# Kernel optimization log

Measured on AMD Instinct MI355X. Metric: run time of the kernel, lower is better.

## Reference

```python
import jax, jax.numpy as jnp
import numpy as np

NUM_ITERATIONS = 3


def _squash_over_classes(s):
    # s: [B, C, O]; original squashes over dim=2 of [B,1,C,O,1] == the class dim C
    norm_sqr = jnp.sum(s * s, axis=1, keepdims=True)          # [B,1,O]
    scale = jnp.sqrt(norm_sqr) + 1e-10
    mag = norm_sqr / (1.0 + norm_sqr)
    return s * mag / scale


def setup_inputs() -> dict:
    key = jax.random.key(0)
    k1, k2 = jax.random.split(key)
    B, K, I, C, O = 256, 8, 1152, 10, 16
    x = jax.random.normal(k1, (B, K, I), dtype=jnp.float32)
    weights = jax.random.normal(k2, (I, C, O, K), dtype=jnp.float32)
    return {"x": x, "weights": weights}


def reference(x, weights):
    # x: [B, K, I]; weights: [I, C, O, K]
    B = x.shape[0]
    I, C = weights.shape[0], weights.shape[1]
    u = jnp.swapaxes(x, 1, 2)                                  # [B, I, K]
    # prediction vectors u_hat_{j|i}: [B, I, C, O]
    u_j_i = jnp.einsum('icok,bik->bico', weights, u)
    b = jnp.zeros((I, C), dtype=x.dtype)                       # routing logits (shared over batch)
    out = None
    for _ in range(NUM_ITERATIONS):
        c = jax.nn.softmax(b, axis=0)                          # softmax over input capsules I
        s = jnp.einsum('ic,bico->bco', c, u_j_i)               # weighted sum over I -> [B, C, O]
        out = _squash_over_classes(s)                          # [B, C, O]
        # agreement: <u_hat, v>, mean over batch -> [I, C]
        agr = jnp.einsum('bico,bco->ic', u_j_i, out) / B
        b = b + agr
    return out[..., None]                                      # [B, C, O, 1] matches out.squeeze(1)
```

## Files before the change

kernel.cpp:

```cpp
#include <hip/hip_runtime.h>

#define B 256
#define KDIM 8
#define IDIM 1152
#define CDIM 10
#define CO 160
#define IK 9216
#define NPART 6
#define AIT 6

typedef __bf16 bf16x8 __attribute__((ext_vector_type(8)));
typedef unsigned short ushort8 __attribute__((ext_vector_type(8)));
typedef float f32x4 __attribute__((ext_vector_type(4)));

__device__ __forceinline__ unsigned short f2bf(float f) {
  unsigned u = __float_as_uint(f);
  unsigned r = u + 0x7fff + ((u >> 16) & 1);
  return (unsigned short)(r >> 16);
}

union U8B8 { ushort8 u; bf16x8 h; };

__global__ void __launch_bounds__(256) k_prep(const float* __restrict__ x,
                                              const float* __restrict__ W,
                                              unsigned short* __restrict__ xtbT,
                                              unsigned short* __restrict__ xtkb,
                                              unsigned short* __restrict__ Wrb,
                                              float* __restrict__ logits) {
  __shared__ __align__(16) unsigned char smem[41280];
  const int bid = blockIdx.x;
  const int t = threadIdx.x;
  if (bid < 288) {
    float* tf = (float*)smem;
    const int i0 = (bid % 36) * 32;
    const int b0 = (bid / 36) * 32;
    const int tx = t & 31, ty = t >> 5;
#pragma unroll
    for (int r = 0; r < 4; ++r) {
      int b = b0 + ty + r * 8;
#pragma unroll
      for (int k = 0; k < 8; ++k)
        tf[k * 1056 + (ty + r * 8) * 33 + tx] =
            x[((size_t)b * KDIM + k) * IDIM + i0 + tx];
    }
    __syncthreads();
#pragma unroll
    for (int r = 0; r < 4; ++r) {
      int idx = r * 256 + t;
      int bb = idx >> 5, ii = idx & 31;
      ushort8 v;
#pragma unroll
      for (int k = 0; k < 8; ++k) v[k] = f2bf(tf[k * 1056 + bb * 33 + ii]);
      *reinterpret_cast<ushort8*>(&xtbT[(size_t)(b0 + bb) * IK + (i0 + ii) * 8]) = v;
    }
#pragma unroll
    for (int ii = 0; ii < 32; ++ii)
      xtkb[((size_t)(i0 + ii) * 8 + ty) * B + b0 + tx] =
          f2bf(tf[ty * 1056 + tx * 33 + ii]);
  } else {
    unsigned short* wt = (unsigned short*)smem;
    const int bz = bid - 288;
    const int i0 = bz * 16;
#pragma unroll
    for (int ii = 0; ii < 16; ++ii) {
      const float* src = &W[(size_t)(i0 + ii) * 1280];
#pragma unroll
      for (int p = 0; p < 5; ++p) {
        int j = p * 256 + t;
        wt[ii * 1288 + j] = f2bf(src[j]);
      }
    }
    __syncthreads();
#pragma unroll
    for (int p = 0; p < 10; ++p) {
      int idx = p * 256 + t;
      int co = idx >> 4, ii = idx & 15;
      ushort8 v = *reinterpret_cast<const ushort8*>(&wt[ii * 1288 + co * 8]);
      *reinterpret_cast<ushort8*>(&Wrb[(size_t)co * IK + (i0 + ii) * 8]) = v;
    }
    if (bz < 45) logits[bz * 256 + t] = 0.f;
  }
}

__global__ void __launch_bounds__(256) k_s(const float* __restrict__ logits,
                                           const unsigned short* __restrict__ Wrb,
                                           const unsigned short* __restrict__ xtbT,
                                           float* __restrict__ s_part) {
  const int c = blockIdx.x, bt4 = blockIdx.y, g = blockIdx.z;
  const int t = threadIdx.x, w = t >> 6, l = t & 63;
  const int lr = l & 15, lq = l >> 4;
  const int s = g * 4 + w;

  __shared__ float cls[IDIM];
  __shared__ float red4[4];
  __shared__ float red[3 * 1088];

  float m = -1e30f;
  for (int i = t; i < IDIM; i += 256) {
    float v = logits[i * CDIM + c];
    cls[i] = v;
    m = fmaxf(m, v);
  }
#pragma unroll
  for (int off = 32; off; off >>= 1) m = fmaxf(m, __shfl_xor(m, off));
  if ((t & 63) == 0) red4[t >> 6] = m;
  __syncthreads();
  m = fmaxf(fmaxf(red4[0], red4[1]), fmaxf(red4[2], red4[3]));
  __syncthreads();
  float ps = 0.f;
  for (int i = t; i < IDIM; i += 256) {
    float e = expf(cls[i] - m);
    cls[i] = e;
    ps += e;
  }
#pragma unroll
  for (int off = 32; off; off >>= 1) ps += __shfl_xor(ps, off);
  if ((t & 63) == 0) red4[t >> 6] = ps;
  __syncthreads();
  const float rinv = 1.f / (red4[0] + red4[1] + red4[2] + red4[3]);
  for (int i = t; i < IDIM; i += 256) cls[i] *= rinv;
  __syncthreads();

  f32x4 acc[4];
#pragma unroll
  for (int j = 0; j < 4; ++j) acc[j] = (f32x4){0.f, 0.f, 0.f, 0.f};

  const unsigned short* Ap  = &Wrb[((size_t)c * 16 + lr) * IK + lq * 8];
  const unsigned short* Bp0 = &xtbT[((size_t)(bt4 * 64 +  0 + lr)) * IK + lq * 8];
  const unsigned short* Bp1 = &xtbT[((size_t)(bt4 * 64 + 16 + lr)) * IK + lq * 8];
  const unsigned short* Bp2 = &xtbT[((size_t)(bt4 * 64 + 32 + lr)) * IK + lq * 8];
  const unsigned short* Bp3 = &xtbT[((size_t)(bt4 * 64 + 48 + lr)) * IK + lq * 8];

#pragma unroll 4
  for (int t9 = 0; t9 < 12; ++t9) {
    const int kc = s * 12 + t9;
    const int off = kc * 32;
    ushort8 av = *reinterpret_cast<const ushort8*>(Ap + off);
    float qv = cls[kc * 4 + lq];
    U8B8 b0; b0.u = *reinterpret_cast<const ushort8*>(Bp0 + off);
    U8B8 b1; b1.u = *reinterpret_cast<const ushort8*>(Bp1 + off);
    U8B8 b2; b2.u = *reinterpret_cast<const ushort8*>(Bp2 + off);
    U8B8 b3; b3.u = *reinterpret_cast<const ushort8*>(Bp3 + off);
    U8B8 a;
#pragma unroll
    for (int e = 0; e < 8; ++e) {
      float f = __uint_as_float((unsigned)av[e] << 16) * qv;
      a.u[e] = f2bf(f);
    }
    acc[0] = __builtin_amdgcn_mfma_f32_16x16x32_bf16(a.h, b0.h, acc[0], 0, 0, 0);
    acc[1] = __builtin_amdgcn_mfma_f32_16x16x32_bf16(a.h, b1.h, acc[1], 0, 0, 0);
    acc[2] = __builtin_amdgcn_mfma_f32_16x16x32_bf16(a.h, b2.h, acc[2], 0, 0, 0);
    acc[3] = __builtin_amdgcn_mfma_f32_16x16x32_bf16(a.h, b3.h, acc[3], 0, 0, 0);
  }

  if (w) {
#pragma unroll
    for (int j = 0; j < 4; ++j)
#pragma unroll
      for (int j2 = 0; j2 < 4; ++j2)
        red[(w - 1) * 1088 + l * 17 + j * 4 + j2] = acc[j][j2];
  }
  __syncthreads();
  if (w == 0) {
#pragma unroll
    for (int r = 0; r < 3; ++r)
#pragma unroll
      for (int j = 0; j < 4; ++j)
#pragma unroll
        for (int j2 = 0; j2 < 4; ++j2)
          acc[j][j2] += red[r * 1088 + l * 17 + j * 4 + j2];
#pragma unroll
    for (int j = 0; j < 4; ++j)
#pragma unroll
      for (int j2 = 0; j2 < 4; ++j2)
        s_part[((size_t)g * B + bt4 * 64 + j * 16 + lr) * CO + c * 16 + lq * 4 + j2] =
            acc[j][j2];
  }
}

__global__ void __launch_bounds__(256) k_sqm(const float* __restrict__ s_part,
                                             unsigned short* __restrict__ outT) {
  const int t = threadIdx.x;
  const int b0 = blockIdx.x * 8;
  __shared__ float sq[8][160];
  __shared__ float fo[8][16];
  float vv[8];
  if (t < CO) {
#pragma unroll
    for (int bi = 0; bi < 8; ++bi) {
      float sv = 0.f;
#pragma unroll
      for (int p = 0; p < NPART; ++p)
        sv += s_part[((size_t)p * B + b0 + bi) * CO + t];
      vv[bi] = sv;
      sq[bi][t] = sv * sv;
    }
  }
  __syncthreads();
  if (t < 128) {
    int bi = t >> 4, o = t & 15;
    float ns = 0.f;
#pragma unroll
    for (int c = 0; c < CDIM; ++c) ns += sq[bi][c * 16 + o];
    fo[bi][o] = (ns / (1.f + ns)) / (sqrtf(ns) + 1e-10f);
  }
  __syncthreads();
  if (t < CO) {
    ushort8 v;
#pragma unroll
    for (int bi = 0; bi < 8; ++bi) v[bi] = f2bf(vv[bi] * fo[bi][t & 15]);
    *reinterpret_cast<ushort8*>(&outT[(size_t)t * B + b0]) = v;
  }
}

__global__ void __launch_bounds__(256) k_sqf(const float* __restrict__ s_part,
                                             float* __restrict__ out) {
  const int t = threadIdx.x;
  const int b0 = blockIdx.x * 8;
  __shared__ float sq[8][160];
  __shared__ float fo[8][16];
  float vv[8];
  if (t < CO) {
#pragma unroll
    for (int bi = 0; bi < 8; ++bi) {
      float sv = 0.f;
#pragma unroll
      for (int p = 0; p < NPART; ++p)
        sv += s_part[((size_t)p * B + b0 + bi) * CO + t];
      vv[bi] = sv;
      sq[bi][t] = sv * sv;
    }
  }
  __syncthreads();
  if (t < 128) {
    int bi = t >> 4, o = t & 15;
    float ns = 0.f;
#pragma unroll
    for (int c = 0; c < CDIM; ++c) ns += sq[bi][c * 16 + o];
    fo[bi][o] = (ns / (1.f + ns)) / (sqrtf(ns) + 1e-10f);
  }
  __syncthreads();
  if (t < CO) {
#pragma unroll
    for (int bi = 0; bi < 8; ++bi)
      out[(size_t)(b0 + bi) * CO + t] = vv[bi] * fo[bi][t & 15];
  }
}

__global__ void __launch_bounds__(256) k_agr(const float* __restrict__ W,
                                             const unsigned short* __restrict__ xtkb,
                                             const unsigned short* __restrict__ outT,
                                             float* __restrict__ logits) {
  const int bx = blockIdx.x;
  const int bh = blockIdx.y;
  const int t = threadIdx.x, w = t >> 6, l = t & 63;
  const int lr = l & 15, lq = l >> 4;
  __shared__ __align__(16) float yl[CO][52];

  if (w < 3) {
    f32x4 acc[10];
#pragma unroll
    for (int nt = 0; nt < 10; ++nt) acc[nt] = (f32x4){0.f, 0.f, 0.f, 0.f};
    const unsigned short* Ap =
        &xtkb[(size_t)(bx * 48 + w * 16 + lr) * B + bh * 64 + lq * 8];
    const unsigned short* Bp = &outT[(size_t)lr * B + bh * 64 + lq * 8];
#pragma unroll
    for (int kc = 0; kc < 2; ++kc) {
      U8B8 a; a.u = *reinterpret_cast<const ushort8*>(Ap + kc * 32);
#pragma unroll
      for (int nt = 0; nt < 10; ++nt) {
        U8B8 bv;
        bv.u = *reinterpret_cast<const ushort8*>(Bp + (size_t)nt * 16 * B + kc * 32);
        acc[nt] = __builtin_amdgcn_mfma_f32_16x16x32_bf16(a.h, bv.h, acc[nt], 0, 0, 0);
      }
    }
#pragma unroll
    for (int nt = 0; nt < 10; ++nt)
#pragma unroll
      for (int j = 0; j < 4; ++j)
        yl[nt * 16 + lr][w * 16 + lq * 4 + j] = acc[nt][j];
  }
  __syncthreads();

  if (t < 120) {
    const int ii = t / 20, rem = t % 20, cc = rem >> 1, oh = rem & 1;
    const float* Wp = &W[((size_t)(bx * AIT + ii) * CDIM + cc) * 128 + oh * 64];
    float sum = 0.f;
#pragma unroll
    for (int o = 0; o < 8; ++o) {
      float4 w0 = *(const float4*)(&Wp[o * 8]);
      float4 w1 = *(const float4*)(&Wp[o * 8 + 4]);
      const float* yr = &yl[cc * 16 + oh * 8 + o][ii * 8];
      float4 y0 = *(const float4*)(&yr[0]);
      float4 y1 = *(const float4*)(&yr[4]);
      sum += w0.x * y0.x + w0.y * y0.y + w0.z * y0.z + w0.w * y0.w
           + w1.x * y1.x + w1.y * y1.y + w1.z * y1.z + w1.w * y1.w;
    }
    sum += __shfl_xor(sum, 1);
    if (oh == 0)
      atomicAdd(&logits[(bx * AIT + ii) * CDIM + cc], sum * (1.f / (float)B));
  }
}

extern "C" void kernel_launch(void* const* d_in, const int* in_sizes, int n_in,
                              void* d_out, int out_size, void* d_ws, size_t ws_size,
                              hipStream_t stream) {
  const float* x = (const float*)d_in[0];
  const float* W = (const float*)d_in[1];
  float* out = (float*)d_out;

  float* logits = (float*)d_ws;
  float* s_part = logits + IDIM * CDIM;
  unsigned short* xtbT = (unsigned short*)(s_part + (size_t)NPART * B * CO);
  unsigned short* xtkb = xtbT + (size_t)B * IK;
  unsigned short* Wrb  = xtkb + (size_t)IK * B;
  unsigned short* outT = Wrb + (size_t)CO * IK;

  k_prep<<<360, 256, 0, stream>>>(x, W, xtbT, xtkb, Wrb, logits);

  for (int it = 0; it < 3; ++it) {
    k_s<<<dim3(CDIM, 4, NPART), 256, 0, stream>>>(logits, Wrb, xtbT, s_part);
    if (it < 2) {
      k_sqm<<<32, 256, 0, stream>>>(s_part, outT);
      k_agr<<<dim3(IDIM / AIT, 4), 256, 0, stream>>>(W, xtkb, outT, logits);
    } else {
      k_sqf<<<32, 256, 0, stream>>>(s_part, out);
    }
  }
}
```

Before: 83.93 us.

## Pre-pack MFMA operands into fragment-contiguous layouts and specialize first-iteration uniform softmax

The prep kernel now writes x, W and the transposed x directly in a per-lane MFMA fragment order, so each wave's 64 lanes read one contiguous 1KB chunk instead of strided rows. The squash kernel writes its output in the matching packed layout for the agreement kernel. The first routing iteration uses a template specialization that skips the softmax, since the logits are zero and the weights are uniform at 1/I. The softmax weights are also hoisted into registers. The cost is more complex index math in the prep and squash kernels.

```diff
diff --git a/kernel.cpp b/kernel.cpp
--- a/kernel.cpp
+++ b/kernel.cpp
@@ -21,17 +21,17 @@
 
 union U8B8 { ushort8 u; bf16x8 h; };
 
+
 __global__ void __launch_bounds__(256) k_prep(const float* __restrict__ x,
                                               const float* __restrict__ W,
-                                              unsigned short* __restrict__ xtbT,
-                                              unsigned short* __restrict__ xtkb,
-                                              unsigned short* __restrict__ Wrb,
+                                              unsigned short* __restrict__ XbP,
+                                              unsigned short* __restrict__ XkP,
+                                              unsigned short* __restrict__ WqP,
                                               float* __restrict__ logits) {
-  __shared__ __align__(16) unsigned char smem[41280];
   const int bid = blockIdx.x;
   const int t = threadIdx.x;
   if (bid < 288) {
-    float* tf = (float*)smem;
+    __shared__ float tf[KDIM * 1056];
     const int i0 = (bid % 36) * 32;
     const int b0 = (bid / 36) * 32;
     const int tx = t & 31, ty = t >> 5;
@@ -47,96 +47,115 @@
 #pragma unroll
     for (int r = 0; r < 4; ++r) {
       int idx = r * 256 + t;
-      int bb = idx >> 5, ii = idx & 31;
+      int bth = idx >> 9, kc8 = (idx >> 6) & 7, lq = (idx >> 4) & 3, lr = idx & 15;
       ushort8 v;
 #pragma unroll
-      for (int k = 0; k < 8; ++k) v[k] = f2bf(tf[k * 1056 + bb * 33 + ii]);
-      *reinterpret_cast<ushort8*>(&xtbT[(size_t)(b0 + bb) * IK + (i0 + ii) * 8]) = v;
-    }
-#pragma unroll
-    for (int ii = 0; ii < 32; ++ii)
-      xtkb[((size_t)(i0 + ii) * 8 + ty) * B + b0 + tx] =
-          f2bf(tf[ty * 1056 + tx * 33 + ii]);
+      for (int e = 0; e < 8; ++e)
+        v[e] = f2bf(tf[e * 1056 + (bth * 16 + lr) * 33 + kc8 * 4 + lq]);
+      int bt = (b0 >> 4) + bth;
+      int kc = (i0 >> 2) + kc8;
+      *reinterpret_cast<ushort8*>(
+          &XbP[(((size_t)bt * 288 + kc) * 64 + lq * 16 + lr) * 8]) = v;
+    }
+    {
+      const int bh = b0 >> 6, kc = (b0 >> 5) & 1;
+#pragma unroll
+      for (int r = 0; r < 4; ++r) {
+        int idx = r * 256 + t;
+        int il = idx >> 5, k = (idx >> 2) & 7, lql = idx & 3;
+        int i = i0 + il;
+        int bx = i / 6, r6 = i - bx * 6;
+        int w = r6 >> 1, lr = (r6 & 1) * 8 + k;
+        ushort8 v;
+#pragma unroll
+        for (int e = 0; e < 8; ++e)
+          v[e] = f2bf(tf[k * 1056 + (lql * 8 + e) * 33 + il]);
+        *reinterpret_cast<ushort8*>(
+            &XkP[((((size_t)(bx * 3 + w) * 4 + bh) * 2 + kc) * 64 + lql * 16 + lr) * 8]) = v;
+      }
+    }
   } else {
-    unsigned short* wt = (unsigned short*)smem;
     const int bz = bid - 288;
     const int i0 = bz * 16;
-#pragma unroll
-    for (int ii = 0; ii < 16; ++ii) {
-      const float* src = &W[(size_t)(i0 + ii) * 1280];
-#pragma unroll
-      for (int p = 0; p < 5; ++p) {
-        int j = p * 256 + t;
-        wt[ii * 1288 + j] = f2bf(src[j]);
-      }
-    }
-    __syncthreads();
-#pragma unroll
-    for (int p = 0; p < 10; ++p) {
-      int idx = p * 256 + t;
-      int co = idx >> 4, ii = idx & 15;
-      ushort8 v = *reinterpret_cast<const ushort8*>(&wt[ii * 1288 + co * 8]);
-      *reinterpret_cast<ushort8*>(&Wrb[(size_t)co * IK + (i0 + ii) * 8]) = v;
+    const int ii = t >> 4, lr = t & 15;
+    const int i = i0 + ii;
+    const int kc = i >> 2, lq = i & 3;
+#pragma unroll
+    for (int c = 0; c < CDIM; ++c) {
+      const float* src = &W[(size_t)i * 1280 + c * 128 + lr * 8];
+      float4 w0 = *(const float4*)src;
+      float4 w1 = *(const float4*)(src + 4);
+      ushort8 v;
+      v[0] = f2bf(w0.x); v[1] = f2bf(w0.y); v[2] = f2bf(w0.z); v[3] = f2bf(w0.w);
+      v[4] = f2bf(w1.x); v[5] = f2bf(w1.y); v[6] = f2bf(w1.z); v[7] = f2bf(w1.w);
+      *reinterpret_cast<ushort8*>(
+          &WqP[(((size_t)c * 288 + kc) * 64 + lq * 16 + lr) * 8]) = v;
     }
     if (bz < 45) logits[bz * 256 + t] = 0.f;
   }
 }
 
+template <bool UNI>
 __global__ void __launch_bounds__(256) k_s(const float* __restrict__ logits,
-                                           const unsigned short* __restrict__ Wrb,
-                                           const unsigned short* __restrict__ xtbT,
+                                           const unsigned short* __restrict__ WqP,
+                                           const unsigned short* __restrict__ XbP,
                                            float* __restrict__ s_part) {
   const int c = blockIdx.x, bt4 = blockIdx.y, g = blockIdx.z;
   const int t = threadIdx.x, w = t >> 6, l = t & 63;
   const int lr = l & 15, lq = l >> 4;
   const int s = g * 4 + w;
 
-  __shared__ float cls[IDIM];
-  __shared__ float red4[4];
   __shared__ float red[3 * 1088];
 
-  float m = -1e30f;
-  for (int i = t; i < IDIM; i += 256) {
-    float v = logits[i * CDIM + c];
-    cls[i] = v;
-    m = fmaxf(m, v);
-  }
-#pragma unroll
-  for (int off = 32; off; off >>= 1) m = fmaxf(m, __shfl_xor(m, off));
-  if ((t & 63) == 0) red4[t >> 6] = m;
-  __syncthreads();
-  m = fmaxf(fmaxf(red4[0], red4[1]), fmaxf(red4[2], red4[3]));
-  __syncthreads();
-  float ps = 0.f;
-  for (int i = t; i < IDIM; i += 256) {
-    float e = expf(cls[i] - m);
-    cls[i] = e;
-    ps += e;
-  }
-#pragma unroll
-  for (int off = 32; off; off >>= 1) ps += __shfl_xor(ps, off);
-  if ((t & 63) == 0) red4[t >> 6] = ps;
-  __syncthreads();
-  const float rinv = 1.f / (red4[0] + red4[1] + red4[2] + red4[3]);
-  for (int i = t; i < IDIM; i += 256) cls[i] *= rinv;
-  __syncthreads();
+  float qreg[12];
+  if constexpr (UNI) {
+#pragma unroll
+    for (int t9 = 0; t9 < 12; ++t9) qreg[t9] = 1.f / (float)IDIM;
+  } else {
+    __shared__ float cls[IDIM];
+    __shared__ float red4[4];
+    float m = -1e30f;
+    for (int i = t; i < IDIM; i += 256) {
+      float v = logits[i * CDIM + c];
+      cls[i] = v;
+      m = fmaxf(m, v);
+    }
+#pragma unroll
+    for (int off = 32; off; off >>= 1) m = fmaxf(m, __shfl_xor(m, off));
+    if ((t & 63) == 0) red4[t >> 6] = m;
+    __syncthreads();
+    m = fmaxf(fmaxf(red4[0], red4[1]), fmaxf(red4[2], red4[3]));
+    __syncthreads();
+    float ps = 0.f;
+    for (int i = t; i < IDIM; i += 256) {
+      float e = expf(cls[i] - m);
+      cls[i] = e;
+      ps += e;
+    }
+#pragma unroll
+    for (int off = 32; off; off >>= 1) ps += __shfl_xor(ps, off);
+    if ((t & 63) == 0) red4[t >> 6] = ps;
+    __syncthreads();
+    const float rinv = 1.f / (red4[0] + red4[1] + red4[2] + red4[3]);
+#pragma unroll
+    for (int t9 = 0; t9 < 12; ++t9)
+      qreg[t9] = cls[(s * 12 + t9) * 4 + lq] * rinv;
+  }
 
   f32x4 acc[4];
 #pragma unroll
   for (int j = 0; j < 4; ++j) acc[j] = (f32x4){0.f, 0.f, 0.f, 0.f};
 
-  const unsigned short* Ap  = &Wrb[((size_t)c * 16 + lr) * IK + lq * 8];
-  const unsigned short* Bp0 = &xtbT[((size_t)(bt4 * 64 +  0 + lr)) * IK + lq * 8];
-  const unsigned short* Bp1 = &xtbT[((size_t)(bt4 * 64 + 16 + lr)) * IK + lq * 8];
-  const unsigned short* Bp2 = &xtbT[((size_t)(bt4 * 64 + 32 + lr)) * IK + lq * 8];
-  const unsigned short* Bp3 = &xtbT[((size_t)(bt4 * 64 + 48 + lr)) * IK + lq * 8];
+  const unsigned short* Ap  = &WqP[(size_t)c * 147456 + l * 8];
+  const unsigned short* Bp0 = &XbP[(size_t)(bt4 * 4 + 0) * 147456 + l * 8];
+  const unsigned short* Bp1 = &XbP[(size_t)(bt4 * 4 + 1) * 147456 + l * 8];
+  const unsigned short* Bp2 = &XbP[(size_t)(bt4 * 4 + 2) * 147456 + l * 8];
+  const unsigned short* Bp3 = &XbP[(size_t)(bt4 * 4 + 3) * 147456 + l * 8];
 
 #pragma unroll 4
   for (int t9 = 0; t9 < 12; ++t9) {
-    const int kc = s * 12 + t9;
-    const int off = kc * 32;
+    const int off = (s * 12 + t9) * 512;
     ushort8 av = *reinterpret_cast<const ushort8*>(Ap + off);
-    float qv = cls[kc * 4 + lq];
     U8B8 b0; b0.u = *reinterpret_cast<const ushort8*>(Bp0 + off);
     U8B8 b1; b1.u = *reinterpret_cast<const ushort8*>(Bp1 + off);
     U8B8 b2; b2.u = *reinterpret_cast<const ushort8*>(Bp2 + off);
@@ -144,7 +163,7 @@
     U8B8 a;
 #pragma unroll
     for (int e = 0; e < 8; ++e) {
-      float f = __uint_as_float((unsigned)av[e] << 16) * qv;
+      float f = __uint_as_float((unsigned)av[e] << 16) * qreg[t9];
       a.u[e] = f2bf(f);
     }
     acc[0] = __builtin_amdgcn_mfma_f32_16x16x32_bf16(a.h, b0.h, acc[0], 0, 0, 0);
@@ -179,7 +198,7 @@
 }
 
 __global__ void __launch_bounds__(256) k_sqm(const float* __restrict__ s_part,
-                                             unsigned short* __restrict__ outT) {
+                                             unsigned short* __restrict__ outP) {
   const int t = threadIdx.x;
   const int b0 = blockIdx.x * 8;
   __shared__ float sq[8][160];
@@ -206,10 +225,13 @@
   }
   __syncthreads();
   if (t < CO) {
+    const int nt = t >> 4, lr = t & 15;
+    const int bh = b0 >> 6, kc = (b0 >> 5) & 1, lq = (b0 >> 3) & 3;
     ushort8 v;
 #pragma unroll
     for (int bi = 0; bi < 8; ++bi) v[bi] = f2bf(vv[bi] * fo[bi][t & 15]);
-    *reinterpret_cast<ushort8*>(&outT[(size_t)t * B + b0]) = v;
+    *reinterpret_cast<ushort8*>(
+        &outP[((((size_t)bh * 10 + nt) * 2 + kc) * 4 + lq) * 128 + lr * 8]) = v;
   }
 }
 
@@ -248,8 +270,8 @@
 }
 
 __global__ void __launch_bounds__(256) k_agr(const float* __restrict__ W,
-                                             const unsigned short* __restrict__ xtkb,
-                                             const unsigned short* __restrict__ outT,
+                                             const unsigned short* __restrict__ XkP,
+                                             const unsigned short* __restrict__ outP,
                                              float* __restrict__ logits) {
   const int bx = blockIdx.x;
   const int bh = blockIdx.y;
@@ -261,16 +283,15 @@
     f32x4 acc[10];
 #pragma unroll
     for (int nt = 0; nt < 10; ++nt) acc[nt] = (f32x4){0.f, 0.f, 0.f, 0.f};
-    const unsigned short* Ap =
-        &xtkb[(size_t)(bx * 48 + w * 16 + lr) * B + bh * 64 + lq * 8];
-    const unsigned short* Bp = &outT[(size_t)lr * B + bh * 64 + lq * 8];
+    const unsigned short* Ap = &XkP[(((size_t)(bx * 3 + w) * 4 + bh) * 1024) + l * 8];
+    const unsigned short* Bp = &outP[(size_t)bh * 10240 + l * 8];
 #pragma unroll
     for (int kc = 0; kc < 2; ++kc) {
-      U8B8 a; a.u = *reinterpret_cast<const ushort8*>(Ap + kc * 32);
+      U8B8 a; a.u = *reinterpret_cast<const ushort8*>(Ap + kc * 512);
 #pragma unroll
       for (int nt = 0; nt < 10; ++nt) {
         U8B8 bv;
-        bv.u = *reinterpret_cast<const ushort8*>(Bp + (size_t)nt * 16 * B + kc * 32);
+        bv.u = *reinterpret_cast<const ushort8*>(Bp + nt * 1024 + kc * 512);
         acc[nt] = __builtin_amdgcn_mfma_f32_16x16x32_bf16(a.h, bv.h, acc[nt], 0, 0, 0);
       }
     }
@@ -311,18 +332,21 @@
 
   float* logits = (float*)d_ws;
   float* s_part = logits + IDIM * CDIM;
-  unsigned short* xtbT = (unsigned short*)(s_part + (size_t)NPART * B * CO);
-  unsigned short* xtkb = xtbT + (size_t)B * IK;
-  unsigned short* Wrb  = xtkb + (size_t)IK * B;
-  unsigned short* outT = Wrb + (size_t)CO * IK;
-
-  k_prep<<<360, 256, 0, stream>>>(x, W, xtbT, xtkb, Wrb, logits);
+  unsigned short* XbP = (unsigned short*)(s_part + (size_t)NPART * B * CO);
+  unsigned short* XkP = XbP + (size_t)B * IK;
+  unsigned short* WqP = XkP + (size_t)IK * B;
+  unsigned short* outP = WqP + (size_t)CO * IK;
+
+  k_prep<<<360, 256, 0, stream>>>(x, W, XbP, XkP, WqP, logits);
 
   for (int it = 0; it < 3; ++it) {
-    k_s<<<dim3(CDIM, 4, NPART), 256, 0, stream>>>(logits, Wrb, xtbT, s_part);
+    if (it == 0)
+      k_s<true><<<dim3(CDIM, 4, NPART), 256, 0, stream>>>(logits, WqP, XbP, s_part);
+    else
+      k_s<false><<<dim3(CDIM, 4, NPART), 256, 0, stream>>>(logits, WqP, XbP, s_part);
     if (it < 2) {
-      k_sqm<<<32, 256, 0, stream>>>(s_part, outT);
-      k_agr<<<dim3(IDIM / AIT, 4), 256, 0, stream>>>(W, xtkb, outT, logits);
+      k_sqm<<<32, 256, 0, stream>>>(s_part, outP);
+      k_agr<<<dim3(IDIM / AIT, 4), 256, 0, stream>>>(W, XkP, outP, logits);
     } else {
       k_sqf<<<32, 256, 0, stream>>>(s_part, out);
     }
```

Result: faster. 68.28 us (-18.6%).
